# Optimization experiments

Hardware: AMD Instinct MI355X
Metric: run time of the kernel (lower is better)

The kernel has to match this reference:

```python
import jax, jax.numpy as jnp
import numpy as np

EPS = 1e-06  # matches SQRegularizer eps


def setup_inputs() -> dict:
    key = jax.random.key(0)
    k1, k2, k3, k4 = jax.random.split(key, 4)
    B, P, S, N = 8, 16, 256, 4096
    surface_points = jax.random.normal(k1, (B, P, S, 3), dtype=jnp.float32)
    points = jax.random.normal(k2, (B, N, 3), dtype=jnp.float32)
    assign_matrix = jax.random.uniform(k3, (B, N, P), dtype=jnp.float32)
    exist = jax.random.uniform(k4, (B, P), dtype=jnp.float32)
    return {
        "surface_points": surface_points,
        "points": points,
        "assign_matrix": assign_matrix,
        "exist": exist,
    }


def reference(surface_points, points, assign_matrix, exist):
    # Squared pairwise distances via ||a||^2 + ||b||^2 - 2 a.b  (== cdist(...)**2)
    a2 = jnp.sum(surface_points * surface_points, axis=-1)          # (B, P, S)
    b2 = jnp.sum(points * points, axis=-1)                          # (B, N)
    cross = jnp.einsum('bpsd,bnd->bpsn', surface_points, points)    # (B, P, S, N)
    d2 = jnp.maximum(a2[..., None] + b2[:, None, None, :] - 2.0 * cross, 0.0)

    # point -> superquadric: min over samples, weighted by soft assignment
    p2s = jnp.min(d2, axis=2)                                       # (B, P, N)
    p2s = jnp.transpose(p2s, (0, 2, 1))                             # (B, N, P)
    point_to_sq = jnp.mean(jnp.mean(jnp.sum(p2s * assign_matrix, axis=-1), axis=-1))

    # superquadric -> point: min over points, mean over samples, existence-weighted
    s2p = jnp.mean(jnp.min(d2, axis=3), axis=-1)                    # (B, P)
    denom = jnp.maximum(jnp.sum(exist, axis=-1), EPS)               # (B,)
    sq_to_point = jnp.mean(jnp.sum(s2p * exist, axis=-1) / denom)

    return point_to_sq + sq_to_point
```

## Files before the change

### kernel.cpp

```cpp
#include <hip/hip_runtime.h>

#define NB 8
#define NP 16
#define NS 256
#define NN 4096
#define NBP (NB*NP)
#define NCHUNK 16
#define CHUNK (NN/NCHUNK)
#define NBLK (NBP*NCHUNK)
#define EPSV 1e-6f

typedef _Float16 half8 __attribute__((ext_vector_type(8)));
typedef float    f32x4 __attribute__((ext_vector_type(4)));

#define H0 ((_Float16)0.0f)
#define H1 ((_Float16)1.0f)



__global__ __launch_bounds__(256, 4) void sqreg_main(
    const float* __restrict__ sp,
    const float* __restrict__ pts,
    const float* __restrict__ assign,
    float* __restrict__ minw,
    float* __restrict__ partials)
{
    __shared__ __align__(16) char smem[4*64*17*4];
    _Float16 (*lsa)[16] = (_Float16(*)[16])smem;
    _Float16 (*lpb)[16] = (_Float16(*)[16])(smem + 8192);
    float    (*pm1t)[64][17] = (float(*)[64][17])smem;
    __shared__ float pm2[4][NS];
    __shared__ float psum[4];

    const int bid   = blockIdx.x;
    const int bp    = bid >> 4;
    const int chunk = bid & 15;
    const int p     = bp & 15;
    const int b     = bp >> 4;
    const int tid   = threadIdx.x;
    const int lane  = tid & 63;
    const int wave  = tid >> 6;
    const int l15   = lane & 15;
    const int lg    = lane >> 4;

    {
        const float* s3 = sp + (size_t)(bp*NS)*3;
        float x = s3[tid*3+0], y = s3[tid*3+1], z = s3[tid*3+2];
        float a2 = x*x + y*y + z*z;
        _Float16 xh=(_Float16)x, yh=(_Float16)y, zh=(_Float16)z, ah=(_Float16)a2;
        _Float16 xl=(_Float16)(x-(float)xh), yl=(_Float16)(y-(float)yh);
        _Float16 zl=(_Float16)(z-(float)zh), al=(_Float16)(a2-(float)ah);
        half8 blo = {xh,xh,xl,yh,yh,yl,zh,zh};
        half8 bhi = {zl,ah,al,H1,H1,H0,H0,H0};
        *(half8*)&lsa[tid][0] = blo;
        *(half8*)&lsa[tid][8] = bhi;

        const float* q3 = pts + (size_t)(b*NN + chunk*CHUNK)*3;
        float bx = q3[tid*3+0], by = q3[tid*3+1], bz = q3[tid*3+2];
        float tx = -2.0f*bx, ty = -2.0f*by, tz = -2.0f*bz;
        float b2 = bx*bx + by*by + bz*bz;
        _Float16 txh=(_Float16)tx, tyh=(_Float16)ty, tzh=(_Float16)tz, bh=(_Float16)b2;
        _Float16 txl=(_Float16)(tx-(float)txh), tyl=(_Float16)(ty-(float)tyh);
        _Float16 tzl=(_Float16)(tz-(float)tzh), bl=(_Float16)(b2-(float)bh);
        half8 alo = {txh,txl,txh,tyh,tyl,tyh,tzh,tzl};
        half8 ahi = {tzh,H1,H1,bh,bl,H0,H0,H0};
        *(half8*)&lpb[tid][0] = alo;
        *(half8*)&lpb[tid][8] = ahi;
    }
    __syncthreads();

    half8 afrag[4];
#pragma unroll
    for (int j = 0; j < 4; ++j) {
        half8 t = {H0,H0,H0,H0,H0,H0,H0,H0};
        if (lane < 32)
            t = *(const half8*)&lpb[wave*64 + j*16 + l15][(lane>>4)*8];
        afrag[j] = t;
    }

    f32x4 rp1[4];
#pragma unroll
    for (int j = 0; j < 4; ++j) rp1[j] = (f32x4){INFINITY,INFINITY,INFINITY,INFINITY};
    float rp2[16];
#pragma unroll
    for (int st = 0; st < 16; ++st) rp2[st] = INFINITY;

#pragma unroll 4
    for (int st = 0; st < 16; ++st) {
        half8 bf = {H0,H0,H0,H0,H0,H0,H0,H0};
        if (lane < 32)
            bf = *(const half8*)&lsa[st*16 + l15][(lane>>4)*8];

        f32x4 acc[4];
#pragma unroll
        for (int j = 0; j < 4; ++j)
            acc[j] = __builtin_amdgcn_mfma_f32_16x16x32_f16(
                afrag[j], bf, (f32x4){0.f,0.f,0.f,0.f}, 0, 0, 0);

        float t0, t1;
#pragma unroll
        for (int j = 0; j < 4; ++j) {
            rp1[j][0] = fminf(rp1[j][0], acc[j][0]);
            rp1[j][1] = fminf(rp1[j][1], acc[j][1]);
            rp1[j][2] = fminf(rp1[j][2], acc[j][2]);
            rp1[j][3] = fminf(rp1[j][3], acc[j][3]);
        }
        t0 = fminf(fminf(acc[0][0], acc[0][1]), fminf(acc[0][2], acc[0][3]));
        t1 = fminf(fminf(acc[1][0], acc[1][1]), fminf(acc[1][2], acc[1][3]));
        t0 = fminf(t0, t1);
        t1 = fminf(fminf(acc[2][0], acc[2][1]), fminf(acc[2][2], acc[2][3]));
        t0 = fminf(t0, t1);
        t1 = fminf(fminf(acc[3][0], acc[3][1]), fminf(acc[3][2], acc[3][3]));
        rp2[st] = fminf(rp2[st], fminf(t0, t1));
    }

    __syncthreads();

#pragma unroll
    for (int st = 0; st < 16; ++st) {
        float v = rp2[st];
        v = fminf(v, __shfl_xor(v, 16, 64));
        v = fminf(v, __shfl_xor(v, 32, 64));
        pm2[wave][st*16 + l15] = v;
    }

#pragma unroll
    for (int j = 0; j < 4; ++j) {
#pragma unroll
        for (int r = 0; r < 4; ++r)
            pm1t[wave][j*16 + lg*4 + r][l15] = rp1[j][r];
    }
    __syncthreads();

    {
        float mm = fminf(fminf(pm2[0][tid], pm2[1][tid]),
                         fminf(pm2[2][tid], pm2[3][tid]));
        minw[(size_t)bid*NS + tid] = fmaxf(mm, 0.0f);
    }
    float acc;
    {
        const float* row = pm1t[tid >> 6][tid & 63];
        float m0 = fminf(fminf(row[0],  row[1]),  fminf(row[2],  row[3]));
        float m1 = fminf(fminf(row[4],  row[5]),  fminf(row[6],  row[7]));
        float m2 = fminf(fminf(row[8],  row[9]),  fminf(row[10], row[11]));
        float m3 = fminf(fminf(row[12], row[13]), fminf(row[14], row[15]));
        float mm = fminf(fminf(m0, m1), fminf(m2, m3));
        acc = fmaxf(mm, 0.0f) *
              assign[(size_t)(b*NN + chunk*CHUNK + tid)*NP + p];
    }
#pragma unroll
    for (int msk = 32; msk >= 1; msk >>= 1)
        acc += __shfl_xor(acc, msk, 64);
    if (lane == 0) psum[wave] = acc;
    __syncthreads();
    if (tid == 0) partials[bid] = psum[0] + psum[1] + psum[2] + psum[3];
}

__global__ __launch_bounds__(256) void sqreg_tail(
    const float* __restrict__ minw,
    const float* __restrict__ partials,
    float* __restrict__ s2p,
    float* __restrict__ pp)
{
    __shared__ float wsum[4];
    const int bp   = blockIdx.x;
    const int tid  = threadIdx.x;
    const int lane = tid & 63;
    const int wave = tid >> 6;

    const float* base = minw + (size_t)(bp*NCHUNK)*NS + tid;
    float m = base[0];
#pragma unroll
    for (int c = 1; c < NCHUNK; ++c) m = fminf(m, base[(size_t)c*NS]);
#pragma unroll
    for (int msk = 32; msk >= 1; msk >>= 1)
        m += __shfl_xor(m, msk, 64);
    if (lane == 0) wsum[wave] = m;
    __syncthreads();

    if (tid == 0) {
        s2p[bp] = (wsum[0] + wsum[1] + wsum[2] + wsum[3]) * (1.0f/(float)NS);
        float a = 0.0f;
#pragma unroll
        for (int c = 0; c < NCHUNK; ++c) a += partials[bp*NCHUNK + c];
        pp[bp] = a;
    }
}

__global__ __launch_bounds__(256) void sqreg_final(
    const float* __restrict__ s2p,
    const float* __restrict__ pp,
    const float* __restrict__ exist,
    float* __restrict__ out)
{
    __shared__ float ppw[2];
    __shared__ float fin[8];
    const int tid = threadIdx.x;

    float tsum = (tid < NBP) ? pp[tid] : 0.0f;
#pragma unroll
    for (int msk = 32; msk >= 1; msk >>= 1)
        tsum += __shfl_xor(tsum, msk, 64);
    if (tid == 0)  ppw[0] = tsum;
    if (tid == 64) ppw[1] = tsum;

    if (tid < NBP) {
        float e  = exist[tid];
        float sv = s2p[tid] * e;
#pragma unroll
        for (int msk = 8; msk >= 1; msk >>= 1) {
            e  += __shfl_xor(e,  msk, 64);
            sv += __shfl_xor(sv, msk, 64);
        }
        if ((tid & 15) == 0) fin[tid >> 4] = sv / fmaxf(e, EPSV);
    }
    __syncthreads();

    if (tid == 0) {
        float sq = 0.0f;
#pragma unroll
        for (int g = 0; g < NB; ++g) sq += fin[g];
        out[0] = (ppw[0] + ppw[1]) / (float)(NB*NN) + sq * (1.0f/(float)NB);
    }
}

extern "C" void kernel_launch(void* const* d_in, const int* in_sizes, int n_in,
                              void* d_out, int out_size, void* d_ws, size_t ws_size,
                              hipStream_t stream) {
    const float* sp     = (const float*)d_in[0];
    const float* pts    = (const float*)d_in[1];
    const float* assign = (const float*)d_in[2];
    const float* exist  = (const float*)d_in[3];
    float* out = (float*)d_out;

    char* ws = (char*)d_ws;
    float* minw = (float*)(ws);
    float* part = (float*)(ws + 0x200000);
    float* s2p  = (float*)(ws + 0x202000);
    float* pp   = (float*)(ws + 0x202400);

    sqreg_main <<<NBLK, 256, 0, stream>>>(sp, pts, assign, minw, part);
    sqreg_tail <<<NBP,  256, 0, stream>>>(minw, part, s2p, pp);
    sqreg_final<<<1,    256, 0, stream>>>(s2p, pp, exist, out);
}
```

Measured before the change: 25.25 us.

## Halve point chunks per block and transpose partial-min layout for vector loads

Each block now processes 512 points instead of 256 (8 chunks instead of 16), doubling MFMA tiles per wave and reusing each staged surface-sample fragment across twice as many point tiles. The per-chunk sample minima are stored transposed so the tail kernel reads them with two float4 loads. This cuts the grid to 1024 blocks, lowers redundant surface-sample staging, and shrinks the intermediate buffer. In exchange it raises register pressure (8 accumulator fragments) and doubles shared memory per block, which may reduce occupancy.

```diff
diff --git a/kernel.cpp b/kernel.cpp
--- a/kernel.cpp
+++ b/kernel.cpp
@@ -5,7 +5,7 @@
 #define NS 256
 #define NN 4096
 #define NBP (NB*NP)
-#define NCHUNK 16
+#define NCHUNK 8
 #define CHUNK (NN/NCHUNK)
 #define NBLK (NBP*NCHUNK)
 #define EPSV 1e-6f
@@ -25,16 +25,16 @@
     float* __restrict__ minw,
     float* __restrict__ partials)
 {
-    __shared__ __align__(16) char smem[4*64*17*4];
+    __shared__ __align__(16) char smem[4*128*17*4];
     _Float16 (*lsa)[16] = (_Float16(*)[16])smem;
     _Float16 (*lpb)[16] = (_Float16(*)[16])(smem + 8192);
-    float    (*pm1t)[64][17] = (float(*)[64][17])smem;
+    float    (*pm1t)[128][17] = (float(*)[128][17])smem;
     __shared__ float pm2[4][NS];
     __shared__ float psum[4];
 
     const int bid   = blockIdx.x;
-    const int bp    = bid >> 4;
-    const int chunk = bid & 15;
+    const int bp    = bid >> 3;
+    const int chunk = bid & 7;
     const int p     = bp & 15;
     const int b     = bp >> 4;
     const int tid   = threadIdx.x;
@@ -56,62 +56,57 @@
         *(half8*)&lsa[tid][8] = bhi;
 
         const float* q3 = pts + (size_t)(b*NN + chunk*CHUNK)*3;
-        float bx = q3[tid*3+0], by = q3[tid*3+1], bz = q3[tid*3+2];
-        float tx = -2.0f*bx, ty = -2.0f*by, tz = -2.0f*bz;
-        float b2 = bx*bx + by*by + bz*bz;
-        _Float16 txh=(_Float16)tx, tyh=(_Float16)ty, tzh=(_Float16)tz, bh=(_Float16)b2;
-        _Float16 txl=(_Float16)(tx-(float)txh), tyl=(_Float16)(ty-(float)tyh);
-        _Float16 tzl=(_Float16)(tz-(float)tzh), bl=(_Float16)(b2-(float)bh);
-        half8 alo = {txh,txl,txh,tyh,tyl,tyh,tzh,tzl};
-        half8 ahi = {tzh,H1,H1,bh,bl,H0,H0,H0};
-        *(half8*)&lpb[tid][0] = alo;
-        *(half8*)&lpb[tid][8] = ahi;
-    }
-    __syncthreads();
-
-    half8 afrag[4];
-#pragma unroll
-    for (int j = 0; j < 4; ++j) {
+#pragma unroll
+        for (int k = 0; k < 2; ++k) {
+            int i = tid + k*256;
+            float bx = q3[i*3+0], by = q3[i*3+1], bz = q3[i*3+2];
+            float tx = -2.0f*bx, ty = -2.0f*by, tz = -2.0f*bz;
+            float b2 = bx*bx + by*by + bz*bz;
+            _Float16 txh=(_Float16)tx, tyh=(_Float16)ty, tzh=(_Float16)tz, bh=(_Float16)b2;
+            _Float16 txl=(_Float16)(tx-(float)txh), tyl=(_Float16)(ty-(float)tyh);
+            _Float16 tzl=(_Float16)(tz-(float)tzh), bl=(_Float16)(b2-(float)bh);
+            half8 alo = {txh,txl,txh,tyh,tyl,tyh,tzh,tzl};
+            half8 ahi = {tzh,H1,H1,bh,bl,H0,H0,H0};
+            *(half8*)&lpb[i][0] = alo;
+            *(half8*)&lpb[i][8] = ahi;
+        }
+    }
+    __syncthreads();
+
+    half8 afrag[8];
+#pragma unroll
+    for (int j = 0; j < 8; ++j) {
         half8 t = {H0,H0,H0,H0,H0,H0,H0,H0};
         if (lane < 32)
-            t = *(const half8*)&lpb[wave*64 + j*16 + l15][(lane>>4)*8];
+            t = *(const half8*)&lpb[wave*128 + j*16 + l15][(lane>>4)*8];
         afrag[j] = t;
     }
 
-    f32x4 rp1[4];
-#pragma unroll
-    for (int j = 0; j < 4; ++j) rp1[j] = (f32x4){INFINITY,INFINITY,INFINITY,INFINITY};
+    f32x4 rp1[8];
+#pragma unroll
+    for (int j = 0; j < 8; ++j) rp1[j] = (f32x4){INFINITY,INFINITY,INFINITY,INFINITY};
     float rp2[16];
 #pragma unroll
     for (int st = 0; st < 16; ++st) rp2[st] = INFINITY;
 
-#pragma unroll 4
+#pragma unroll 2
     for (int st = 0; st < 16; ++st) {
         half8 bf = {H0,H0,H0,H0,H0,H0,H0,H0};
         if (lane < 32)
             bf = *(const half8*)&lsa[st*16 + l15][(lane>>4)*8];
 
-        f32x4 acc[4];
-#pragma unroll
-        for (int j = 0; j < 4; ++j)
-            acc[j] = __builtin_amdgcn_mfma_f32_16x16x32_f16(
+        float tmin = INFINITY;
+#pragma unroll
+        for (int j = 0; j < 8; ++j) {
+            f32x4 acc = __builtin_amdgcn_mfma_f32_16x16x32_f16(
                 afrag[j], bf, (f32x4){0.f,0.f,0.f,0.f}, 0, 0, 0);
-
-        float t0, t1;
-#pragma unroll
-        for (int j = 0; j < 4; ++j) {
-            rp1[j][0] = fminf(rp1[j][0], acc[j][0]);
-            rp1[j][1] = fminf(rp1[j][1], acc[j][1]);
-            rp1[j][2] = fminf(rp1[j][2], acc[j][2]);
-            rp1[j][3] = fminf(rp1[j][3], acc[j][3]);
+            rp1[j][0] = fminf(rp1[j][0], acc[0]);
+            rp1[j][1] = fminf(rp1[j][1], acc[1]);
+            rp1[j][2] = fminf(rp1[j][2], acc[2]);
+            rp1[j][3] = fminf(rp1[j][3], acc[3]);
+            tmin = fminf(tmin, fminf(fminf(acc[0], acc[1]), fminf(acc[2], acc[3])));
         }
-        t0 = fminf(fminf(acc[0][0], acc[0][1]), fminf(acc[0][2], acc[0][3]));
-        t1 = fminf(fminf(acc[1][0], acc[1][1]), fminf(acc[1][2], acc[1][3]));
-        t0 = fminf(t0, t1);
-        t1 = fminf(fminf(acc[2][0], acc[2][1]), fminf(acc[2][2], acc[2][3]));
-        t0 = fminf(t0, t1);
-        t1 = fminf(fminf(acc[3][0], acc[3][1]), fminf(acc[3][2], acc[3][3]));
-        rp2[st] = fminf(rp2[st], fminf(t0, t1));
+        rp2[st] = fminf(rp2[st], tmin);
     }
 
     __syncthreads();
@@ -125,7 +120,7 @@
     }
 
 #pragma unroll
-    for (int j = 0; j < 4; ++j) {
+    for (int j = 0; j < 8; ++j) {
 #pragma unroll
         for (int r = 0; r < 4; ++r)
             pm1t[wave][j*16 + lg*4 + r][l15] = rp1[j][r];
@@ -135,18 +130,20 @@
     {
         float mm = fminf(fminf(pm2[0][tid], pm2[1][tid]),
                          fminf(pm2[2][tid], pm2[3][tid]));
-        minw[(size_t)bid*NS + tid] = fmaxf(mm, 0.0f);
-    }
-    float acc;
-    {
-        const float* row = pm1t[tid >> 6][tid & 63];
+        minw[(size_t)(bp*NS + tid)*NCHUNK + chunk] = fmaxf(mm, 0.0f);
+    }
+    float acc = 0.0f;
+#pragma unroll
+    for (int u = 0; u < 2; ++u) {
+        int n = tid + u*256;
+        const float* row = pm1t[n >> 7][n & 127];
         float m0 = fminf(fminf(row[0],  row[1]),  fminf(row[2],  row[3]));
         float m1 = fminf(fminf(row[4],  row[5]),  fminf(row[6],  row[7]));
         float m2 = fminf(fminf(row[8],  row[9]),  fminf(row[10], row[11]));
         float m3 = fminf(fminf(row[12], row[13]), fminf(row[14], row[15]));
         float mm = fminf(fminf(m0, m1), fminf(m2, m3));
-        acc = fmaxf(mm, 0.0f) *
-              assign[(size_t)(b*NN + chunk*CHUNK + tid)*NP + p];
+        acc += fmaxf(mm, 0.0f) *
+               assign[(size_t)(b*NN + chunk*CHUNK + n)*NP + p];
     }
 #pragma unroll
     for (int msk = 32; msk >= 1; msk >>= 1)
@@ -168,10 +165,10 @@
     const int lane = tid & 63;
     const int wave = tid >> 6;
 
-    const float* base = minw + (size_t)(bp*NCHUNK)*NS + tid;
-    float m = base[0];
-#pragma unroll
-    for (int c = 1; c < NCHUNK; ++c) m = fminf(m, base[(size_t)c*NS]);
+    const f32x4* base = (const f32x4*)(minw + (size_t)(bp*NS + tid)*NCHUNK);
+    f32x4 v0 = base[0], v1 = base[1];
+    float m = fminf(fminf(fminf(v0[0], v0[1]), fminf(v0[2], v0[3])),
+                    fminf(fminf(v1[0], v1[1]), fminf(v1[2], v1[3])));
 #pragma unroll
     for (int msk = 32; msk >= 1; msk >>= 1)
         m += __shfl_xor(m, msk, 64);
@@ -235,9 +232,9 @@
 
     char* ws = (char*)d_ws;
     float* minw = (float*)(ws);
-    float* part = (float*)(ws + 0x200000);
-    float* s2p  = (float*)(ws + 0x202000);
-    float* pp   = (float*)(ws + 0x202400);
+    float* part = (float*)(ws + 0x100000);
+    float* s2p  = (float*)(ws + 0x101000);
+    float* pp   = (float*)(ws + 0x101200);
 
     sqreg_main <<<NBLK, 256, 0, stream>>>(sp, pts, assign, minw, part);
     sqreg_tail <<<NBP,  256, 0, stream>>>(minw, part, s2p, pp);
```

New measurement: 24.67 us. 1.02x faster.
